# Kernel optimization log

Measured on AMD Instinct MI355X. Metric: run time of the kernel, lower is better.

The kernel has to match this reference:

```python
import jax, jax.numpy as jnp
import numpy as np

EPS = 1e-5
NEG_SLOPE = 0.01  # F.leaky_relu default


def setup_inputs() -> dict:
    key = jax.random.key(0)
    k1, k2, k3, k4 = jax.random.split(key, 4)
    N, F, H = 8192, 512, 2
    inputs = jax.random.normal(k1, (N, F), dtype=jnp.float32)
    adj = jnp.zeros((N, N), dtype=jnp.float32)  # accepted but unused by the module
    # torch Linear(F, F*H, bias=False): y = x @ W with W of shape [F, F*H]
    W = jax.random.normal(k2, (F, F * H), dtype=jnp.float32) * (1.0 / np.sqrt(F))
    a_w = jax.random.normal(k3, (1,), dtype=jnp.float32)  # Linear(1,1) weight
    a_b = jax.random.normal(k4, (1,), dtype=jnp.float32)  # Linear(1,1) bias
    return {"inputs": inputs, "adj": adj, "W": W, "a_w": a_w, "a_b": a_b}


def reference(inputs, adj, W, a_w, a_b):
    # Wh, Ws = chunk(inputs @ W, 2)
    WhWs = inputs @ W                       # [N, 2F]
    Wh, Ws = jnp.split(WhWs, 2, axis=-1)    # each [N, F]
    # bias = a(ones) = a_w * 1 + a_b  (constant scalar broadcast)
    bias = (a_w + a_b)[0]
    # dense attention: tanh(Wh + Ws + bias) @ Wh^T  -> [N, N]
    scores = jnp.tanh(Wh + Ws + bias) @ Wh.T
    attn = jax.nn.softmax(scores, axis=-1)  # [N, N]
    out = attn @ Wh + inputs                # [N, F] residual
    # training-mode batch norm over node dim, no affine
    mean = jnp.mean(out, axis=0)
    var = jnp.var(out, axis=0)
    out = (out - mean) * jax.lax.rsqrt(var + EPS)
    return jnp.where(out >= 0, out, NEG_SLOPE * out)
```

## Files before the change

### kernel.cpp

```cpp
#include <hip/hip_runtime.h>

using f32x4 = float    __attribute__((ext_vector_type(4)));
using f16x8 = _Float16 __attribute__((ext_vector_type(8)));
using f16x4 = _Float16 __attribute__((ext_vector_type(4)));

__device__ __forceinline__ void gload_lds16(const void* g, void* l) {
    __builtin_amdgcn_global_load_lds(
        (__attribute__((address_space(1))) void*)(void*)g,
        (__attribute__((address_space(3))) void*)l, 16, 0, 0);
}


__global__ __launch_bounds__(256) void k_cvt_x(
    const float* __restrict__ in, _Float16* __restrict__ out) {
    int i = (blockIdx.x * 256 + threadIdx.x) * 8;
    f32x4 a = *(const f32x4*)(in + i);
    f32x4 b = *(const f32x4*)(in + i + 4);
    f16x8 o;
    #pragma unroll
    for (int j = 0; j < 4; ++j) { o[j] = (_Float16)a[j]; o[j + 4] = (_Float16)b[j]; }
    *(f16x8*)(out + i) = o;
}

__global__ __launch_bounds__(256) void k_cvtT(
    const float* __restrict__ in, _Float16* __restrict__ out, int R, int C) {
    __shared__ _Float16 tile[32][33];
    int c0 = blockIdx.x * 32, r0 = blockIdx.y * 32;
    int tx = threadIdx.x & 31, ty = threadIdx.x >> 5;
    #pragma unroll
    for (int i = ty; i < 32; i += 8)
        tile[i][tx] = (_Float16)in[(size_t)(r0 + i) * C + c0 + tx];
    __syncthreads();
    #pragma unroll
    for (int i = ty; i < 32; i += 8)
        out[(size_t)(c0 + i) * R + r0 + tx] = tile[tx][i];
}

__global__ __launch_bounds__(512, 4) void k_gemm1f(
    const _Float16* __restrict__ A, const _Float16* __restrict__ Bt,
    _Float16* __restrict__ Whh, _Float16* __restrict__ T,
    _Float16* __restrict__ WhT,
    const float* __restrict__ aw, const float* __restrict__ ab) {
    __shared__ _Float16 As[128 * 32];
    __shared__ _Float16 B0s[64 * 32];
    __shared__ _Float16 B1s[64 * 32];
    const float bias = aw[0] + ab[0];
    const int row0 = blockIdx.y * 128, col0 = blockIdx.x * 64;
    const int tid = threadIdx.x, w = tid >> 6, lane = tid & 63;
    const int wm = w >> 2, wn = w & 3;
    const int lrow = lane & 15, quad = lane >> 4;
    const int r16 = lane >> 2;
    const int kc = (((lane & 3) - ((lane >> 3) & 3)) & 3) * 8;
    const int sq = ((quad + ((lrow >> 1) & 3)) & 3) * 8;
    f32x4 acc0[4] = {}, acc1[4] = {};
    for (int k0 = 0; k0 < 512; k0 += 32) {
        gload_lds16(A + (size_t)(row0 + w * 16 + r16) * 512 + k0 + kc,
                    As + w * 512);
        if (w < 4)
            gload_lds16(Bt + (size_t)(col0 + w * 16 + r16) * 512 + k0 + kc,
                        B0s + w * 512);
        else
            gload_lds16(Bt + (size_t)(col0 + 512 + (w - 4) * 16 + r16) * 512 + k0 + kc,
                        B1s + (w - 4) * 512);
        __syncthreads();
        f16x8 af[4], b0, b1;
        #pragma unroll
        for (int i = 0; i < 4; ++i)
            af[i] = *(const f16x8*)(As + (wm * 64 + i * 16 + lrow) * 32 + sq);
        b0 = *(const f16x8*)(B0s + (wn * 16 + lrow) * 32 + sq);
        b1 = *(const f16x8*)(B1s + (wn * 16 + lrow) * 32 + sq);
        #pragma unroll
        for (int mi = 0; mi < 4; ++mi) {
            acc0[mi] = __builtin_amdgcn_mfma_f32_16x16x32_f16(af[mi], b0, acc0[mi], 0, 0, 0);
            acc1[mi] = __builtin_amdgcn_mfma_f32_16x16x32_f16(af[mi], b1, acc1[mi], 0, 0, 0);
        }
        __syncthreads();
    }
    const int col = col0 + wn * 16 + lrow;
    #pragma unroll
    for (int mi = 0; mi < 4; ++mi) {
        int rowb = row0 + wm * 64 + mi * 16 + quad * 4;
        f16x4 pw;
        #pragma unroll
        for (int r = 0; r < 4; ++r) {
            float wh = acc0[mi][r];
            float tt = tanhf(wh + acc1[mi][r] + bias);
            Whh[(size_t)(rowb + r) * 512 + col] = (_Float16)wh;
            T[(size_t)(rowb + r) * 512 + col]   = (_Float16)tt;
            pw[r] = (_Float16)wh;
        }
        *(f16x4*)(WhT + (size_t)col * 8192 + rowb) = pw;
    }
}

__global__ __launch_bounds__(512, 4) void k_gemm2(
    const _Float16* __restrict__ A,
    const _Float16* __restrict__ Bt,
    _Float16* __restrict__ Cp) {
    __shared__ _Float16 As[256 * 64];
    __shared__ _Float16 Bs[128 * 64];
    const int row0 = blockIdx.y * 256, col0 = blockIdx.x * 128;
    const int tid = threadIdx.x, w = tid >> 6, lane = tid & 63;
    const int wm = w >> 1, wn = w & 1;
    const int lrow = lane & 15, quad = lane >> 4;
    const int r8 = lane >> 3;
    const int kc8 = (((lane & 7) - r8) & 7) * 8;
    f32x4 acc[4][4] = {};
    for (int k0 = 0; k0 < 512; k0 += 64) {
        #pragma unroll
        for (int i = 0; i < 6; ++i) {
            int c = w + i * 8;
            if (c < 32) {
                gload_lds16(A + (size_t)(row0 + c * 8 + r8) * 512 + k0 + kc8,
                            As + c * 512);
            } else {
                int c2 = c - 32;
                gload_lds16(Bt + (size_t)(col0 + c2 * 8 + r8) * 512 + k0 + kc8,
                            Bs + c2 * 512);
            }
        }
        __syncthreads();
        #pragma unroll
        for (int ks = 0; ks < 2; ++ks) {
            const int sl = ((quad + ks * 4 + lrow) & 7) * 8;
            f16x8 af[4], bf[4];
            #pragma unroll
            for (int i = 0; i < 4; ++i)
                af[i] = *(const f16x8*)(As + (wm * 64 + i * 16 + lrow) * 64 + sl);
            #pragma unroll
            for (int i = 0; i < 4; ++i)
                bf[i] = *(const f16x8*)(Bs + (wn * 64 + i * 16 + lrow) * 64 + sl);
            #pragma unroll
            for (int mi = 0; mi < 4; ++mi)
                #pragma unroll
                for (int ni = 0; ni < 4; ++ni)
                    acc[mi][ni] = __builtin_amdgcn_mfma_f32_16x16x32_f16(
                        af[mi], bf[ni], acc[mi][ni], 0, 0, 0);
        }
        __syncthreads();
    }
    #pragma unroll
    for (int mi = 0; mi < 4; ++mi) {
        #pragma unroll
        for (int ni = 0; ni < 4; ++ni) {
            int col = col0 + wn * 64 + ni * 16 + lrow;
            #pragma unroll
            for (int r = 0; r < 4; ++r) {
                int row = row0 + wm * 64 + mi * 16 + quad * 4 + r;
                Cp[(size_t)row * 8192 + col] = (_Float16)acc[mi][ni][r];
            }
        }
    }
}

__global__ __launch_bounds__(256) void k_softmax_rows(
    _Float16* __restrict__ S, int N) {
    const int row = blockIdx.x;
    _Float16* prow = S + (size_t)row * N;
    const int t = threadIdx.x;
    float v[32];
    #pragma unroll
    for (int it = 0; it < 4; ++it) {
        f16x8 h = *(const f16x8*)(prow + (it * 256 + t) * 8);
        #pragma unroll
        for (int j = 0; j < 8; ++j) v[it * 8 + j] = (float)h[j];
    }
    float m = v[0];
    #pragma unroll
    for (int j = 1; j < 32; ++j) m = fmaxf(m, v[j]);
    #pragma unroll
    for (int off = 32; off > 0; off >>= 1) m = fmaxf(m, __shfl_xor(m, off));
    __shared__ float red[8];
    const int wid = t >> 6, lane = t & 63;
    if (lane == 0) red[wid] = m;
    __syncthreads();
    m = fmaxf(fmaxf(red[0], red[1]), fmaxf(red[2], red[3]));
    float l = 0.f;
    #pragma unroll
    for (int j = 0; j < 32; ++j) { v[j] = __expf(v[j] - m); l += v[j]; }
    #pragma unroll
    for (int off = 32; off > 0; off >>= 1) l += __shfl_xor(l, off);
    if (lane == 0) red[4 + wid] = l;
    __syncthreads();
    float rl = 1.f / (red[4] + red[5] + red[6] + red[7]);
    #pragma unroll
    for (int it = 0; it < 4; ++it) {
        f16x8 pk;
        #pragma unroll
        for (int j = 0; j < 8; ++j)
            pk[j] = (_Float16)(v[it * 8 + j] * rl);
        *(f16x8*)(prow + (it * 256 + t) * 8) = pk;
    }
}

__global__ __launch_bounds__(512, 4) void k_gemm3(
    const _Float16* __restrict__ A,
    const _Float16* __restrict__ Bt,
    float* __restrict__ Cp) {
    __shared__ _Float16 As[128 * 64];
    __shared__ _Float16 Bs[256 * 64];
    const int bid = blockIdx.x;
    const int orig = ((bid & 7) << 6) | (bid >> 3);
    const int bx = orig & 1, by = (orig >> 1) & 63, bz = orig >> 7;
    const int row0 = by * 128, col0 = bx * 256;
    const size_t zoff = (size_t)bz * 2048;
    Cp += (size_t)bz * ((size_t)8192 * 512);
    const int tid = threadIdx.x, w = tid >> 6, lane = tid & 63;
    const int wm = w >> 2, wn = w & 3;
    const int lrow = lane & 15, quad = lane >> 4;
    const int r8 = lane >> 3;
    const int kc8 = (((lane & 7) - r8) & 7) * 8;
    f32x4 acc[4][4] = {};
    for (int k0 = 0; k0 < 2048; k0 += 64) {
        #pragma unroll
        for (int i = 0; i < 6; ++i) {
            int c = w + i * 8;
            if (c < 16) {
                gload_lds16(A + (size_t)(row0 + c * 8 + r8) * 8192 + zoff + k0 + kc8,
                            As + c * 512);
            } else {
                int c2 = c - 16;
                gload_lds16(Bt + (size_t)(col0 + c2 * 8 + r8) * 8192 + zoff + k0 + kc8,
                            Bs + c2 * 512);
            }
        }
        __syncthreads();
        #pragma unroll
        for (int ks = 0; ks < 2; ++ks) {
            const int sl = ((quad + ks * 4 + lrow) & 7) * 8;
            f16x8 af[4], bf[4];
            #pragma unroll
            for (int i = 0; i < 4; ++i)
                af[i] = *(const f16x8*)(As + (wm * 64 + i * 16 + lrow) * 64 + sl);
            #pragma unroll
            for (int i = 0; i < 4; ++i)
                bf[i] = *(const f16x8*)(Bs + (wn * 64 + i * 16 + lrow) * 64 + sl);
            #pragma unroll
            for (int mi = 0; mi < 4; ++mi)
                #pragma unroll
                for (int ni = 0; ni < 4; ++ni)
                    acc[mi][ni] = __builtin_amdgcn_mfma_f32_16x16x32_f16(
                        af[mi], bf[ni], acc[mi][ni], 0, 0, 0);
        }
        __syncthreads();
    }
    #pragma unroll
    for (int mi = 0; mi < 4; ++mi) {
        #pragma unroll
        for (int ni = 0; ni < 4; ++ni) {
            int col = col0 + wn * 64 + ni * 16 + lrow;
            #pragma unroll
            for (int r = 0; r < 4; ++r) {
                int row = row0 + wm * 64 + mi * 16 + quad * 4 + r;
                Cp[(size_t)row * 512 + col] = acc[mi][ni][r];
            }
        }
    }
}

__global__ __launch_bounds__(256) void k_reduce_stats(
    const float* __restrict__ part, const float* __restrict__ X,
    float* __restrict__ outf, float* __restrict__ cs, float* __restrict__ cq) {
    const int t = threadIdx.x;
    const int r0 = blockIdx.x * 32;
    constexpr size_t PS = (size_t)8192 * 512;
    float s0 = 0, q0 = 0, s1 = 0, q1 = 0;
    for (int r = 0; r < 32; ++r) {
        size_t base = (size_t)(r0 + r) * 512;
        float a = part[base + t] + part[PS + base + t]
                + part[2 * PS + base + t] + part[3 * PS + base + t] + X[base + t];
        float b = part[base + t + 256] + part[PS + base + t + 256]
                + part[2 * PS + base + t + 256] + part[3 * PS + base + t + 256]
                + X[base + t + 256];
        outf[base + t] = a;       outf[base + t + 256] = b;
        s0 += a; q0 += a * a; s1 += b; q1 += b * b;
    }
    atomicAdd(&cs[t], s0);       atomicAdd(&cq[t], q0);
    atomicAdd(&cs[t + 256], s1); atomicAdd(&cq[t + 256], q1);
}

__global__ __launch_bounds__(256) void k_bn_lrelu(
    const float* __restrict__ outf, const float* __restrict__ colsum,
    const float* __restrict__ colsq, float* __restrict__ out) {
    int i = (blockIdx.x * 256 + threadIdx.x) * 4;
    int c = i & 511;
    constexpr float rN = 1.f / 8192.f;
    f32x4 v = *(const f32x4*)(outf + i);
    f32x4 s = *(const f32x4*)(colsum + c);
    f32x4 q = *(const f32x4*)(colsq + c);
    f32x4 y;
    #pragma unroll
    for (int j = 0; j < 4; ++j) {
        float mean = s[j] * rN;
        float var  = q[j] * rN - mean * mean;
        float t = (v[j] - mean) * rsqrtf(var + 1e-5f);
        y[j] = (t >= 0.f) ? t : 0.01f * t;
    }
    *(f32x4*)(out + i) = y;
}

extern "C" void kernel_launch(void* const* d_in, const int* in_sizes, int n_in,
                              void* d_out, int out_size, void* d_ws, size_t ws_size,
                              hipStream_t stream) {
    const float* X  = (const float*)d_in[0];
    const float* W  = (const float*)d_in[2];
    const float* aw = (const float*)d_in[3];
    const float* ab = (const float*)d_in[4];
    float* out = (float*)d_out;

    char* ws = (char*)d_ws;
    _Float16* Xh   = (_Float16*)(ws + 0x0);
    _Float16* Wt   = (_Float16*)(ws + 0x800000);
    _Float16* T    = (_Float16*)(ws + 0x900000);
    _Float16* Whh  = (_Float16*)(ws + 0x1100000);
    _Float16* WhT  = (_Float16*)(ws + 0x1900000);
    _Float16* S    = (_Float16*)(ws + 0x2100000);
    float*    outf = (float*)   (ws + 0xA100000);
    float*    part = (float*)   (ws + 0xB100000);
    float*    cs   = (float*)   (ws + 0xF100000);
    float*    cq   = (float*)   (ws + 0xF100800);

    hipMemsetAsync(cs, 0, 4096, stream);
    k_cvt_x<<<dim3((8192 * 512) / 2048), 256, 0, stream>>>(X, Xh);
    k_cvtT<<<dim3(1024 / 32, 512 / 32), 256, 0, stream>>>(W, Wt, 512, 1024);
    k_gemm1f<<<dim3(8, 64), 512, 0, stream>>>(Xh, Wt, Whh, T, WhT, aw, ab);
    k_gemm2<<<dim3(64, 32), 512, 0, stream>>>(T, Whh, S);
    k_softmax_rows<<<dim3(8192), 256, 0, stream>>>(S, 8192);
    k_gemm3<<<dim3(512), 512, 0, stream>>>(S, WhT, part);
    k_reduce_stats<<<dim3(256), 256, 0, stream>>>(part, X, outf, cs, cq);
    k_bn_lrelu<<<dim3((8192 * 512) / 1024), 256, 0, stream>>>(outf, cs, cq, out);
}
```

Measured before the change: 511.8 us.

## Double-buffer LDS in score and PV GEMMs with k-step 32 pipelining

Both large GEMM kernels now split their LDS tiles into two buffers of K=32 and issue the async global-to-LDS loads for the next slice before running MFMAs on the current one. This overlaps memory latency with compute and cuts barriers from two per 64-wide step to one per 32-wide step. The LDS swizzle and load mapping are adjusted for the 32-wide rows. The cost is more barriers per unit of K and fewer MFMAs per barrier.

```diff
diff --git a/kernel.cpp b/kernel.cpp
--- a/kernel.cpp
+++ b/kernel.cpp
@@ -97,48 +97,56 @@
     const _Float16* __restrict__ A,
     const _Float16* __restrict__ Bt,
     _Float16* __restrict__ Cp) {
-    __shared__ _Float16 As[256 * 64];
-    __shared__ _Float16 Bs[128 * 64];
+    __shared__ _Float16 As[2 * 256 * 32];
+    __shared__ _Float16 Bs[2 * 128 * 32];
     const int row0 = blockIdx.y * 256, col0 = blockIdx.x * 128;
     const int tid = threadIdx.x, w = tid >> 6, lane = tid & 63;
     const int wm = w >> 1, wn = w & 1;
     const int lrow = lane & 15, quad = lane >> 4;
-    const int r8 = lane >> 3;
-    const int kc8 = (((lane & 7) - r8) & 7) * 8;
+    const int r16 = lane >> 2;
+    const int kc = (((lane & 3) - ((lane >> 3) & 3)) & 3) * 8;
+    const int sq = ((quad + ((lrow >> 1) & 3)) & 3) * 8;
     f32x4 acc[4][4] = {};
-    for (int k0 = 0; k0 < 512; k0 += 64) {
-        #pragma unroll
-        for (int i = 0; i < 6; ++i) {
-            int c = w + i * 8;
-            if (c < 32) {
-                gload_lds16(A + (size_t)(row0 + c * 8 + r8) * 512 + k0 + kc8,
-                            As + c * 512);
-            } else {
-                int c2 = c - 32;
-                gload_lds16(Bt + (size_t)(col0 + c2 * 8 + r8) * 512 + k0 + kc8,
-                            Bs + c2 * 512);
-            }
-        }
-        __syncthreads();
-        #pragma unroll
-        for (int ks = 0; ks < 2; ++ks) {
-            const int sl = ((quad + ks * 4 + lrow) & 7) * 8;
-            f16x8 af[4], bf[4];
+    auto stage = [&](int b, int k0) {
+        _Float16* as = As + b * (256 * 32);
+        _Float16* bs = Bs + b * (128 * 32);
+        #pragma unroll
+        for (int i = 0; i < 3; ++i) {
+            int cc = w + i * 8;
+            if (cc < 16)
+                gload_lds16(A + (size_t)(row0 + cc * 16 + r16) * 512 + k0 + kc,
+                            as + cc * 512);
+            else
+                gload_lds16(Bt + (size_t)(col0 + (cc - 16) * 16 + r16) * 512 + k0 + kc,
+                            bs + (cc - 16) * 512);
+        }
+    };
+    auto compute = [&](int b) {
+        const _Float16* as = As + b * (256 * 32);
+        const _Float16* bs = Bs + b * (128 * 32);
+        f16x8 af[4], bf[4];
+        #pragma unroll
+        for (int i = 0; i < 4; ++i)
+            af[i] = *(const f16x8*)(as + (wm * 64 + i * 16 + lrow) * 32 + sq);
+        #pragma unroll
+        for (int i = 0; i < 4; ++i)
+            bf[i] = *(const f16x8*)(bs + (wn * 64 + i * 16 + lrow) * 32 + sq);
+        #pragma unroll
+        for (int mi = 0; mi < 4; ++mi)
             #pragma unroll
-            for (int i = 0; i < 4; ++i)
-                af[i] = *(const f16x8*)(As + (wm * 64 + i * 16 + lrow) * 64 + sl);
-            #pragma unroll
-            for (int i = 0; i < 4; ++i)
-                bf[i] = *(const f16x8*)(Bs + (wn * 64 + i * 16 + lrow) * 64 + sl);
-            #pragma unroll
-            for (int mi = 0; mi < 4; ++mi)
-                #pragma unroll
-                for (int ni = 0; ni < 4; ++ni)
-                    acc[mi][ni] = __builtin_amdgcn_mfma_f32_16x16x32_f16(
-                        af[mi], bf[ni], acc[mi][ni], 0, 0, 0);
-        }
-        __syncthreads();
-    }
+            for (int ni = 0; ni < 4; ++ni)
+                acc[mi][ni] = __builtin_amdgcn_mfma_f32_16x16x32_f16(
+                    af[mi], bf[ni], acc[mi][ni], 0, 0, 0);
+    };
+    stage(0, 0);
+    __syncthreads();
+    #pragma unroll 1
+    for (int t = 1; t < 15; t += 2) {
+        stage(1, t * 32);       compute(0); __syncthreads();
+        stage(0, (t + 1) * 32); compute(1); __syncthreads();
+    }
+    stage(1, 15 * 32); compute(0); __syncthreads();
+    compute(1);
     #pragma unroll
     for (int mi = 0; mi < 4; ++mi) {
         #pragma unroll
@@ -197,8 +205,8 @@
     const _Float16* __restrict__ A,
     const _Float16* __restrict__ Bt,
     float* __restrict__ Cp) {
-    __shared__ _Float16 As[128 * 64];
-    __shared__ _Float16 Bs[256 * 64];
+    __shared__ _Float16 As[2 * 128 * 32];
+    __shared__ _Float16 Bs[2 * 256 * 32];
     const int bid = blockIdx.x;
     const int orig = ((bid & 7) << 6) | (bid >> 3);
     const int bx = orig & 1, by = (orig >> 1) & 63, bz = orig >> 7;
@@ -208,42 +216,50 @@
     const int tid = threadIdx.x, w = tid >> 6, lane = tid & 63;
     const int wm = w >> 2, wn = w & 3;
     const int lrow = lane & 15, quad = lane >> 4;
-    const int r8 = lane >> 3;
-    const int kc8 = (((lane & 7) - r8) & 7) * 8;
+    const int r16 = lane >> 2;
+    const int kc = (((lane & 3) - ((lane >> 3) & 3)) & 3) * 8;
+    const int sq = ((quad + ((lrow >> 1) & 3)) & 3) * 8;
     f32x4 acc[4][4] = {};
-    for (int k0 = 0; k0 < 2048; k0 += 64) {
-        #pragma unroll
-        for (int i = 0; i < 6; ++i) {
-            int c = w + i * 8;
-            if (c < 16) {
-                gload_lds16(A + (size_t)(row0 + c * 8 + r8) * 8192 + zoff + k0 + kc8,
-                            As + c * 512);
-            } else {
-                int c2 = c - 16;
-                gload_lds16(Bt + (size_t)(col0 + c2 * 8 + r8) * 8192 + zoff + k0 + kc8,
-                            Bs + c2 * 512);
-            }
-        }
-        __syncthreads();
-        #pragma unroll
-        for (int ks = 0; ks < 2; ++ks) {
-            const int sl = ((quad + ks * 4 + lrow) & 7) * 8;
-            f16x8 af[4], bf[4];
+    auto stage = [&](int b, int k0) {
+        _Float16* as = As + b * (128 * 32);
+        _Float16* bs = Bs + b * (256 * 32);
+        #pragma unroll
+        for (int i = 0; i < 3; ++i) {
+            int cc = w + i * 8;
+            if (cc < 8)
+                gload_lds16(A + (size_t)(row0 + cc * 16 + r16) * 8192 + zoff + k0 + kc,
+                            as + cc * 512);
+            else
+                gload_lds16(Bt + (size_t)(col0 + (cc - 8) * 16 + r16) * 8192 + zoff + k0 + kc,
+                            bs + (cc - 8) * 512);
+        }
+    };
+    auto compute = [&](int b) {
+        const _Float16* as = As + b * (128 * 32);
+        const _Float16* bs = Bs + b * (256 * 32);
+        f16x8 af[4], bf[4];
+        #pragma unroll
+        for (int i = 0; i < 4; ++i)
+            af[i] = *(const f16x8*)(as + (wm * 64 + i * 16 + lrow) * 32 + sq);
+        #pragma unroll
+        for (int i = 0; i < 4; ++i)
+            bf[i] = *(const f16x8*)(bs + (wn * 64 + i * 16 + lrow) * 32 + sq);
+        #pragma unroll
+        for (int mi = 0; mi < 4; ++mi)
             #pragma unroll
-            for (int i = 0; i < 4; ++i)
-                af[i] = *(const f16x8*)(As + (wm * 64 + i * 16 + lrow) * 64 + sl);
-            #pragma unroll
-            for (int i = 0; i < 4; ++i)
-                bf[i] = *(const f16x8*)(Bs + (wn * 64 + i * 16 + lrow) * 64 + sl);
-            #pragma unroll
-            for (int mi = 0; mi < 4; ++mi)
-                #pragma unroll
-                for (int ni = 0; ni < 4; ++ni)
-                    acc[mi][ni] = __builtin_amdgcn_mfma_f32_16x16x32_f16(
-                        af[mi], bf[ni], acc[mi][ni], 0, 0, 0);
-        }
-        __syncthreads();
-    }
+            for (int ni = 0; ni < 4; ++ni)
+                acc[mi][ni] = __builtin_amdgcn_mfma_f32_16x16x32_f16(
+                    af[mi], bf[ni], acc[mi][ni], 0, 0, 0);
+    };
+    stage(0, 0);
+    __syncthreads();
+    #pragma unroll 1
+    for (int t = 1; t < 63; t += 2) {
+        stage(1, t * 32);       compute(0); __syncthreads();
+        stage(0, (t + 1) * 32); compute(1); __syncthreads();
+    }
+    stage(1, 63 * 32); compute(0); __syncthreads();
+    compute(1);
     #pragma unroll
     for (int mi = 0; mi < 4; ++mi) {
         #pragma unroll
```

Result: slower. 525.8 us (+2.7%).
